# Kernel optimization log

Hardware: AMD Instinct MI355X
Metric: run time of the kernel (lower is better)

The kernel has to match this reference:

```python
import jax, jax.numpy as jnp
import numpy as np

N_NODES = 50000
N_EDGES = 800000
N_FEAT = 128
N_HID = 128
N_CLS = 40
BN_EPS = 1e-5


def setup_inputs() -> dict:
    key = jax.random.key(0)
    ks = jax.random.split(key, 8)
    return {
        "x": jax.random.normal(ks[0], (N_NODES, N_FEAT), dtype=jnp.float32),
        "edge_index": jax.random.randint(ks[1], (2, N_EDGES), 0, N_NODES, dtype=jnp.int64),
        "W1l": jax.random.normal(ks[2], (N_HID, N_FEAT), dtype=jnp.float32) / np.sqrt(N_FEAT),
        "b1": jnp.zeros((N_HID,), dtype=jnp.float32),
        "W1r": jax.random.normal(ks[3], (N_HID, N_FEAT), dtype=jnp.float32) / np.sqrt(N_FEAT),
        "gamma": jnp.ones((N_HID,), dtype=jnp.float32),
        "beta": jnp.zeros((N_HID,), dtype=jnp.float32),
        "run_mean": jax.random.normal(ks[4], (N_HID,), dtype=jnp.float32) * 0.1,
        "run_var": jax.random.uniform(ks[5], (N_HID,), dtype=jnp.float32) + 0.5,
        "W2l": jax.random.normal(ks[6], (N_CLS, N_HID), dtype=jnp.float32) / np.sqrt(N_HID),
        "b2": jnp.zeros((N_CLS,), dtype=jnp.float32),
        "W2r": jax.random.normal(ks[7], (N_CLS, N_HID), dtype=jnp.float32) / np.sqrt(N_HID),
    }


def _sage_conv(h, src, dst, n_nodes, inv_deg, Wl, bl, Wr):
    # mean-aggregate neighbor features at each destination node
    agg = jax.ops.segment_sum(h[src], dst, num_segments=n_nodes)  # [N, D]
    agg = agg * inv_deg[:, None]
    # PyG SAGEConv: lin_l(aggr) (with bias) + lin_r(x) (no bias)
    return agg @ Wl.T + bl + h @ Wr.T


def reference(x, edge_index, W1l, b1, W1r, gamma, beta, run_mean, run_var, W2l, b2, W2r):
    src, dst = edge_index[0], edge_index[1]
    n = x.shape[0]
    deg = jax.ops.segment_sum(jnp.ones_like(src, dtype=x.dtype), dst, num_segments=n)
    inv_deg = 1.0 / jnp.maximum(deg, 1.0)
    h = _sage_conv(x, src, dst, n, inv_deg, W1l, b1, W1r)
    # transition: ReLU -> BatchNorm1d (eval: running stats) -> Dropout (identity in eval)
    h = jnp.maximum(h, 0.0)
    h = (h - run_mean) * (gamma / jnp.sqrt(run_var + BN_EPS)) + beta
    out = _sage_conv(h, src, dst, n, inv_deg, W2l, b2, W2r)
    return out
```

## Files before the change

### kernel.cpp

```cpp
#include <hip/hip_runtime.h>

#define N_NODES 50000
#define N_EDGES 800000
#define N_FEAT 128
#define N_HID 128
#define N_CLS 40
#define BN_EPS 1e-5f

#define CSR_STRIDE 64
#define NXCD 8
#define P_NODES 6250
#define CSR_B 2048
#define CSR_BO 256
#define WPACK_B 84
#define XPACK_B 3125
#define G2_SUB 51

typedef short bf16x8 __attribute__((ext_vector_type(8)));
typedef float f32x4 __attribute__((ext_vector_type(4)));

__device__ __forceinline__ unsigned bfpack(float a, float b) {
    unsigned ua = __float_as_uint(a), ub = __float_as_uint(b);
    ua = (ua + 0x7FFFu + ((ua >> 16) & 1u)) >> 16;
    ub = (ub + 0x7FFFu + ((ub >> 16) & 1u)) >> 16;
    return ua | (ub << 16);
}
__device__ __forceinline__ unsigned short bfr1(float a) {
    unsigned u = __float_as_uint(a);
    u = (u + 0x7FFFu + ((u >> 16) & 1u)) >> 16;
    return (unsigned short)u;
}
__device__ __forceinline__ float bflo(unsigned u) { return __uint_as_float(u << 16); }
__device__ __forceinline__ float bfhi(unsigned u) { return __uint_as_float(u & 0xFFFF0000u); }

__global__ __launch_bounds__(256) void degprep_kernel(
    const int* __restrict__ src, const int* __restrict__ dst,
    int* __restrict__ deg_i, unsigned short* __restrict__ csr_pad,
    const float* __restrict__ W1l, const float* __restrict__ W1r,
    const float* __restrict__ W2l, const float* __restrict__ W2r,
    const float* __restrict__ x, unsigned* __restrict__ WfA,
    unsigned* __restrict__ WfB, unsigned* __restrict__ x_bf16) {
    int b = blockIdx.x;
    int t = threadIdx.x;
    if (b < CSR_B) {
        const int p = b & (NXCD - 1);
        const int bo = b >> 3;
        const int plo = p * P_NODES;
        const int phi = plo + P_NODES;
        const int4* dst4 = (const int4*)dst;
        const int4* src4 = (const int4*)src;
        for (int c = bo; c * 1024 < N_EDGES; c += CSR_BO) {
            int e = c * 1024 + t * 4;
            if (e < N_EDGES) {
                int i4 = e >> 2;
                int4 d4 = dst4[i4];
                bool k0 = (d4.x >= plo) && (d4.x < phi);
                bool k1 = (d4.y >= plo) && (d4.y < phi);
                bool k2 = (d4.z >= plo) && (d4.z < phi);
                bool k3 = (d4.w >= plo) && (d4.w < phi);
                if (k0 | k1 | k2 | k3) {
                    int4 s4 = src4[i4];
                    if (k0) { int r = atomicAdd(&deg_i[d4.x], 1);
                        if (r < CSR_STRIDE) csr_pad[d4.x * CSR_STRIDE + r] = (unsigned short)s4.x; }
                    if (k1) { int r = atomicAdd(&deg_i[d4.y], 1);
                        if (r < CSR_STRIDE) csr_pad[d4.y * CSR_STRIDE + r] = (unsigned short)s4.y; }
                    if (k2) { int r = atomicAdd(&deg_i[d4.z], 1);
                        if (r < CSR_STRIDE) csr_pad[d4.z * CSR_STRIDE + r] = (unsigned short)s4.z; }
                    if (k3) { int r = atomicAdd(&deg_i[d4.w], 1);
                        if (r < CSR_STRIDE) csr_pad[d4.w * CSR_STRIDE + r] = (unsigned short)s4.w; }
                }
            }
        }
        return;
    }
    int i = (b - CSR_B) * 256 + t;
    if (b < CSR_B + WPACK_B) {
        if (i < 16384) {
            int f = i >> 8, r = i & 255;
            int lane = r >> 2, u = r & 3;
            int phase = f >> 5, kc = (f >> 3) & 3, nt = f & 7;
            int k0 = phase * 128 + kc * 32 + (lane >> 4) * 8 + u * 2;
            int n = nt * 16 + (lane & 15);
            float w0, w1;
            if (k0 < 128) {
                w0 = W1l[n * 128 + k0];
                w1 = W1l[n * 128 + k0 + 1];
            } else {
                w0 = W1r[n * 128 + k0 - 128];
                w1 = W1r[n * 128 + k0 - 127];
            }
            WfA[i] = bfpack(w0, w1);
        } else if (i < 21504) {
            int j = i - 16384;
            int f = j >> 8, r = j & 255;
            int lane = r >> 2, u = r & 3;
            int kc = f / 5, nt = f % 5;
            int k0 = kc * 32 + (lane >> 4) * 8 + u * 2;
            int n = nt * 16 + (lane & 15);
            float w0, w1;
            if (n < 40) {
                w0 = W2l[n * 128 + k0];
                w1 = W2l[n * 128 + k0 + 1];
            } else {
                w0 = W2r[(n - 40) * 128 + k0];
                w1 = W2r[(n - 40) * 128 + k0 + 1];
            }
            WfB[j] = bfpack(w0, w1);
        }
    } else {
        int j = (b - CSR_B - WPACK_B) * 256 + t;
        if (j < 800000) {
            const float4* xf = (const float4*)x;
            float4 a = xf[(size_t)j * 2];
            float4 bq = xf[(size_t)j * 2 + 1];
            uint4 o;
            o.x = bfpack(a.x, a.y);
            o.y = bfpack(a.z, a.w);
            o.z = bfpack(bq.x, bq.y);
            o.w = bfpack(bq.z, bq.w);
            ((uint4*)x_bf16)[j] = o;
        }
    }
}

__global__ __launch_bounds__(256) void gg_kernel(
    const unsigned short* __restrict__ csr_pad, const int* __restrict__ deg_i,
    const unsigned* __restrict__ x_bf16,
    const unsigned* __restrict__ WfA, const unsigned* __restrict__ WfB,
    const float* __restrict__ b1,
    const float* __restrict__ gamma, const float* __restrict__ beta,
    const float* __restrict__ rmean, const float* __restrict__ rvar,
    unsigned short* __restrict__ z2s, float* __restrict__ p2) {
    __shared__ unsigned Asu0[16 * 68];
    __shared__ unsigned Asu1[16 * 68];
    __shared__ __align__(16) unsigned short Cs[16 * 64];
    const int t = threadIdx.x;
    const int wid = __builtin_amdgcn_readfirstlane(t >> 6);
    const int lane = t & 63;
    const int li = lane & 15;
    const int quad = lane >> 4;
    const int sg = t >> 4;
    const int gl = t & 15;
    const int tb = blockIdx.x * 16;
    const uint4* xb4 = (const uint4*)x_bf16;

    uint4 xs = xb4[(size_t)(tb + sg) * 16 + gl];
    ((uint2*)Cs)[t] = ((const uint2*)(csr_pad + (size_t)tb * 64))[t];
    __syncthreads();

    int gid = tb + sg;
    int n = min(deg_i[gid], CSR_STRIDE);
    const unsigned short* cr = Cs + sg * 64;
    float acc[8];
#pragma unroll
    for (int j = 0; j < 8; ++j) acc[j] = 0.f;
    int k = 0;
    for (; k + 7 < n; k += 8) {
        uint4 tv[8];
#pragma unroll
        for (int q = 0; q < 8; ++q) {
            int s = cr[k + q];
            tv[q] = xb4[(size_t)s * 16 + gl];
        }
#pragma unroll
        for (int q = 0; q < 8; ++q) {
            acc[0] += bflo(tv[q].x); acc[1] += bfhi(tv[q].x);
            acc[2] += bflo(tv[q].y); acc[3] += bfhi(tv[q].y);
            acc[4] += bflo(tv[q].z); acc[5] += bfhi(tv[q].z);
            acc[6] += bflo(tv[q].w); acc[7] += bfhi(tv[q].w);
        }
    }
    if (k + 3 < n) {
        uint4 tv[4];
#pragma unroll
        for (int q = 0; q < 4; ++q) {
            int s = cr[k + q];
            tv[q] = xb4[(size_t)s * 16 + gl];
        }
#pragma unroll
        for (int q = 0; q < 4; ++q) {
            acc[0] += bflo(tv[q].x); acc[1] += bfhi(tv[q].x);
            acc[2] += bflo(tv[q].y); acc[3] += bfhi(tv[q].y);
            acc[4] += bflo(tv[q].z); acc[5] += bfhi(tv[q].z);
            acc[6] += bflo(tv[q].w); acc[7] += bfhi(tv[q].w);
        }
        k += 4;
    }
    for (; k < n; ++k) {
        int s = cr[k];
        uint4 t0 = xb4[(size_t)s * 16 + gl];
        acc[0] += bflo(t0.x); acc[1] += bfhi(t0.x);
        acc[2] += bflo(t0.y); acc[3] += bfhi(t0.y);
        acc[4] += bflo(t0.z); acc[5] += bfhi(t0.z);
        acc[6] += bflo(t0.w); acc[7] += bfhi(t0.w);
    }
    float inv = 1.0f / fmaxf((float)n, 1.0f);
    uint4 o;
    o.x = bfpack(acc[0] * inv, acc[1] * inv);
    o.y = bfpack(acc[2] * inv, acc[3] * inv);
    o.z = bfpack(acc[4] * inv, acc[5] * inv);
    o.w = bfpack(acc[6] * inv, acc[7] * inv);

    *(uint4*)&Asu1[sg * 68 + gl * 4] = xs;
    *(uint4*)&Asu0[sg * 68 + gl * 4] = o;
    __syncthreads();

    bf16x8 af0[4], af1[4];
#pragma unroll
    for (int kc = 0; kc < 4; ++kc) {
        af0[kc] = *(const bf16x8*)&Asu0[li * 68 + kc * 16 + quad * 4];
        af1[kc] = *(const bf16x8*)&Asu1[li * 68 + kc * 16 + quad * 4];
    }

    f32x4 dacc[2];
#pragma unroll
    for (int j = 0; j < 2; ++j) dacc[j] = (f32x4){0.f, 0.f, 0.f, 0.f};
#pragma unroll
    for (int j = 0; j < 2; ++j) {
        int nt = wid * 2 + j;
#pragma unroll
        for (int kc = 0; kc < 4; ++kc) {
            bf16x8 bfr = *(const bf16x8*)(WfA + (size_t)(kc * 8 + nt) * 256 + lane * 4);
            dacc[j] = __builtin_amdgcn_mfma_f32_16x16x32_bf16(af0[kc], bfr, dacc[j], 0, 0, 0);
        }
#pragma unroll
        for (int kc = 0; kc < 4; ++kc) {
            bf16x8 bfr = *(const bf16x8*)(WfA + 8192 + (size_t)(kc * 8 + nt) * 256 + lane * 4);
            dacc[j] = __builtin_amdgcn_mfma_f32_16x16x32_bf16(af1[kc], bfr, dacc[j], 0, 0, 0);
        }
    }
    __syncthreads();

    unsigned short* Hs = (unsigned short*)Asu0;
#pragma unroll
    for (int j = 0; j < 2; ++j) {
        int nt = wid * 2 + j;
        int cgc = nt * 16 + li;
        float sc = gamma[cgc] * rsqrtf(rvar[cgc] + BN_EPS);
        float sh = fmaf(-rmean[cgc], sc, beta[cgc]);
        float bb = b1[cgc];
#pragma unroll
        for (int r = 0; r < 4; ++r) {
            int row = quad * 4 + r;
            float pre = dacc[j][r] + bb;
            Hs[row * 136 + cgc] = bfr1(fmaf(fmaxf(pre, 0.f), sc, sh));
        }
    }
    __syncthreads();

    bf16x8 af2[4];
#pragma unroll
    for (int kc = 0; kc < 4; ++kc)
        af2[kc] = *(const bf16x8*)&Asu0[li * 68 + kc * 16 + quad * 4];

    int nNT = (wid == 0) ? 2 : 1;
    f32x4 d2[2];
#pragma unroll
    for (int j = 0; j < 2; ++j) d2[j] = (f32x4){0.f, 0.f, 0.f, 0.f};
    for (int j = 0; j < nNT; ++j) {
        int nt = (j == 0) ? wid : 4;
#pragma unroll
        for (int kc = 0; kc < 4; ++kc) {
            bf16x8 bfr = *(const bf16x8*)(WfB + (size_t)(kc * 5 + nt) * 256 + lane * 4);
            d2[j] = __builtin_amdgcn_mfma_f32_16x16x32_bf16(af2[kc], bfr, d2[j], 0, 0, 0);
        }
    }
    for (int j = 0; j < nNT; ++j) {
        int nt = (j == 0) ? wid : 4;
        int cgc = nt * 16 + li;
#pragma unroll
        for (int r = 0; r < 4; ++r) {
            int row = tb + quad * 4 + r;
            float vv = d2[j][r];
            if (cgc < 40) z2s[(size_t)row * 40 + cgc] = bfr1(vv);
            else p2[(size_t)row * 40 + (cgc - 40)] = vv;
        }
    }
}

__global__ __launch_bounds__(256) void gather2_kernel(const unsigned short* __restrict__ csr_pad,
                                                      const int* __restrict__ deg_i,
                                                      const unsigned short* __restrict__ z2s,
                                                      const float* __restrict__ p2,
                                                      const float* __restrict__ b2,
                                                      float* __restrict__ out) {
    __shared__ __align__(16) unsigned short Cs[G2_SUB * 64];
    int t = threadIdx.x;
    int nb_base = blockIdx.x * G2_SUB;
    int nn = min(G2_SUB, N_NODES - nb_base);
    int limit_u2 = (nn * 64) >> 2;
    const uint2* cg = (const uint2*)(csr_pad + (size_t)nb_base * 64);
    for (int i = t; i < limit_u2; i += 256) ((uint2*)Cs)[i] = cg[i];
    __syncthreads();

    int sub = t / 5;
    int li = t - sub * 5;
    if (sub >= G2_SUB) return;
    int gid = nb_base + sub;
    if (gid >= N_NODES) return;
    int n = min(deg_i[gid], CSR_STRIDE);
    const unsigned short* cr = Cs + sub * 64;
    const uint4* z4 = (const uint4*)z2s;
    float acc[8];
#pragma unroll
    for (int j = 0; j < 8; ++j) acc[j] = 0.f;
    int k = 0;
    for (; k + 7 < n; k += 8) {
        uint4 tv[8];
#pragma unroll
        for (int q = 0; q < 8; ++q) {
            int s = cr[k + q];
            tv[q] = z4[(size_t)s * 5 + li];
        }
#pragma unroll
        for (int q = 0; q < 8; ++q) {
            acc[0] += bflo(tv[q].x); acc[1] += bfhi(tv[q].x);
            acc[2] += bflo(tv[q].y); acc[3] += bfhi(tv[q].y);
            acc[4] += bflo(tv[q].z); acc[5] += bfhi(tv[q].z);
            acc[6] += bflo(tv[q].w); acc[7] += bfhi(tv[q].w);
        }
    }
    if (k + 3 < n) {
        uint4 tv[4];
#pragma unroll
        for (int q = 0; q < 4; ++q) {
            int s = cr[k + q];
            tv[q] = z4[(size_t)s * 5 + li];
        }
#pragma unroll
        for (int q = 0; q < 4; ++q) {
            acc[0] += bflo(tv[q].x); acc[1] += bfhi(tv[q].x);
            acc[2] += bflo(tv[q].y); acc[3] += bfhi(tv[q].y);
            acc[4] += bflo(tv[q].z); acc[5] += bfhi(tv[q].z);
            acc[6] += bflo(tv[q].w); acc[7] += bfhi(tv[q].w);
        }
        k += 4;
    }
    for (; k < n; ++k) {
        int s = cr[k];
        uint4 t0 = z4[(size_t)s * 5 + li];
        acc[0] += bflo(t0.x); acc[1] += bfhi(t0.x);
        acc[2] += bflo(t0.y); acc[3] += bfhi(t0.y);
        acc[4] += bflo(t0.z); acc[5] += bfhi(t0.z);
        acc[6] += bflo(t0.w); acc[7] += bfhi(t0.w);
    }
    float inv = 1.0f / fmaxf((float)n, 1.0f);
    const float4* p4 = (const float4*)p2;
    const float4* b4 = (const float4*)b2;
    float4 pa = p4[(size_t)gid * 10 + li * 2];
    float4 pb = p4[(size_t)gid * 10 + li * 2 + 1];
    float4 ba = b4[li * 2];
    float4 bb = b4[li * 2 + 1];
    float4 ra, rb;
    ra.x = fmaf(acc[0], inv, pa.x + ba.x);
    ra.y = fmaf(acc[1], inv, pa.y + ba.y);
    ra.z = fmaf(acc[2], inv, pa.z + ba.z);
    ra.w = fmaf(acc[3], inv, pa.w + ba.w);
    rb.x = fmaf(acc[4], inv, pb.x + bb.x);
    rb.y = fmaf(acc[5], inv, pb.y + bb.y);
    rb.z = fmaf(acc[6], inv, pb.z + bb.z);
    rb.w = fmaf(acc[7], inv, pb.w + bb.w);
    ((float4*)out)[(size_t)gid * 10 + li * 2] = ra;
    ((float4*)out)[(size_t)gid * 10 + li * 2 + 1] = rb;
}

extern "C" void kernel_launch(void* const* d_in, const int* in_sizes, int n_in,
                              void* d_out, int out_size, void* d_ws, size_t ws_size,
                              hipStream_t stream) {
    const float* x     = (const float*)d_in[0];
    const int*   ei    = (const int*)d_in[1];
    const float* W1l   = (const float*)d_in[2];
    const float* b1    = (const float*)d_in[3];
    const float* W1r   = (const float*)d_in[4];
    const float* gamma = (const float*)d_in[5];
    const float* beta  = (const float*)d_in[6];
    const float* rmean = (const float*)d_in[7];
    const float* rvar  = (const float*)d_in[8];
    const float* W2l   = (const float*)d_in[9];
    const float* b2    = (const float*)d_in[10];
    const float* W2r   = (const float*)d_in[11];
    float* out = (float*)d_out;

    int* deg_i              = (int*)d_ws;
    unsigned short* csr_pad = (unsigned short*)(deg_i + 50048);
    unsigned* WfA           = (unsigned*)(deg_i + 50048 + 1600000);
    unsigned* WfB           = WfA + 16384;
    unsigned* x_bf16        = WfB + 5120;
    unsigned short* z2s     = (unsigned short*)(x_bf16 + 3200000);
    float* p2               = (float*)(z2s + (size_t)50048 * 40);

    const int* src = ei;
    const int* dst = ei + N_EDGES;

    hipMemsetAsync(deg_i, 0, (size_t)50048 * sizeof(int), stream);

    degprep_kernel<<<CSR_B + WPACK_B + XPACK_B, 256, 0, stream>>>(
        src, dst, deg_i, csr_pad, W1l, W1r, W2l, W2r, x, WfA, WfB, x_bf16);

    gg_kernel<<<N_NODES / 16, 256, 0, stream>>>(
        csr_pad, deg_i, x_bf16, WfA, WfB, b1, gamma, beta, rmean, rvar, z2s, p2);

    gather2_kernel<<<(N_NODES + G2_SUB - 1) / G2_SUB, 256, 0, stream>>>(
        csr_pad, deg_i, z2s, p2, b2, out);
}
```

Baseline: 182.9 us.

## Build padded CSR via two-pass bucketed scatter with LDS-local atomics

Replaces the per-XCD-partitioned global-atomic CSR build with a two-phase approach. Edges are first bucketed by dst>>8 into 196 fixed-capacity record buffers using shared-memory histograms and one global atomic per bucket per block. A second kernel then builds each bucket's 256-node CSR slice in LDS and writes it out coalesced. The aim is to cut the global atomic traffic and scattered 2-byte writes, at the cost of an extra kernel launch, an intermediate record buffer, and a fixed bucket capacity that silently drops edges if a bucket overflows.

```diff
diff --git a/kernel.cpp b/kernel.cpp
--- a/kernel.cpp
+++ b/kernel.cpp
@@ -8,12 +8,12 @@
 #define BN_EPS 1e-5f
 
 #define CSR_STRIDE 64
-#define NXCD 8
-#define P_NODES 6250
-#define CSR_B 2048
-#define CSR_BO 256
-#define WPACK_B 84
-#define XPACK_B 3125
+#define NBKT 196
+#define REC_CAP 6144
+#define PA_B 196
+#define WPACK1K 21
+#define XPACK1K 782
+#define D1_B (PA_B + WPACK1K + XPACK1K)
 #define G2_SUB 51
 
 typedef short bf16x8 __attribute__((ext_vector_type(8)));
@@ -33,48 +33,50 @@
 __device__ __forceinline__ float bflo(unsigned u) { return __uint_as_float(u << 16); }
 __device__ __forceinline__ float bfhi(unsigned u) { return __uint_as_float(u & 0xFFFF0000u); }
 
-__global__ __launch_bounds__(256) void degprep_kernel(
+__global__ __launch_bounds__(1024) void d1_kernel(
     const int* __restrict__ src, const int* __restrict__ dst,
-    int* __restrict__ deg_i, unsigned short* __restrict__ csr_pad,
+    int* __restrict__ gcur, unsigned* __restrict__ rec,
     const float* __restrict__ W1l, const float* __restrict__ W1r,
     const float* __restrict__ W2l, const float* __restrict__ W2r,
     const float* __restrict__ x, unsigned* __restrict__ WfA,
     unsigned* __restrict__ WfB, unsigned* __restrict__ x_bf16) {
     int b = blockIdx.x;
     int t = threadIdx.x;
-    if (b < CSR_B) {
-        const int p = b & (NXCD - 1);
-        const int bo = b >> 3;
-        const int plo = p * P_NODES;
-        const int phi = plo + P_NODES;
-        const int4* dst4 = (const int4*)dst;
-        const int4* src4 = (const int4*)src;
-        for (int c = bo; c * 1024 < N_EDGES; c += CSR_BO) {
-            int e = c * 1024 + t * 4;
-            if (e < N_EDGES) {
-                int i4 = e >> 2;
-                int4 d4 = dst4[i4];
-                bool k0 = (d4.x >= plo) && (d4.x < phi);
-                bool k1 = (d4.y >= plo) && (d4.y < phi);
-                bool k2 = (d4.z >= plo) && (d4.z < phi);
-                bool k3 = (d4.w >= plo) && (d4.w < phi);
-                if (k0 | k1 | k2 | k3) {
-                    int4 s4 = src4[i4];
-                    if (k0) { int r = atomicAdd(&deg_i[d4.x], 1);
-                        if (r < CSR_STRIDE) csr_pad[d4.x * CSR_STRIDE + r] = (unsigned short)s4.x; }
-                    if (k1) { int r = atomicAdd(&deg_i[d4.y], 1);
-                        if (r < CSR_STRIDE) csr_pad[d4.y * CSR_STRIDE + r] = (unsigned short)s4.y; }
-                    if (k2) { int r = atomicAdd(&deg_i[d4.z], 1);
-                        if (r < CSR_STRIDE) csr_pad[d4.z * CSR_STRIDE + r] = (unsigned short)s4.z; }
-                    if (k3) { int r = atomicAdd(&deg_i[d4.w], 1);
-                        if (r < CSR_STRIDE) csr_pad[d4.w * CSR_STRIDE + r] = (unsigned short)s4.w; }
-                }
+    if (b < PA_B) {
+        __shared__ int hist[NBKT];
+        __shared__ int base[NBKT];
+        if (t < NBKT) hist[t] = 0;
+        __syncthreads();
+        int e = b * 4096 + t * 4;
+        bool val = e < N_EDGES;
+        int4 d4 = {0, 0, 0, 0}, s4 = {0, 0, 0, 0};
+        int bk[4], rk[4];
+        if (val) {
+            d4 = ((const int4*)dst)[e >> 2];
+            s4 = ((const int4*)src)[e >> 2];
+            bk[0] = d4.x >> 8; rk[0] = atomicAdd(&hist[bk[0]], 1);
+            bk[1] = d4.y >> 8; rk[1] = atomicAdd(&hist[bk[1]], 1);
+            bk[2] = d4.z >> 8; rk[2] = atomicAdd(&hist[bk[2]], 1);
+            bk[3] = d4.w >> 8; rk[3] = atomicAdd(&hist[bk[3]], 1);
+        }
+        __syncthreads();
+        if (t < NBKT) base[t] = atomicAdd(&gcur[t], hist[t]);
+        __syncthreads();
+        if (val) {
+            int dl[4] = {d4.x & 255, d4.y & 255, d4.z & 255, d4.w & 255};
+            int sv[4] = {s4.x, s4.y, s4.z, s4.w};
+#pragma unroll
+            for (int q = 0; q < 4; ++q) {
+                int pos = base[bk[q]] + rk[q];
+                if (pos < REC_CAP)
+                    rec[(size_t)bk[q] * REC_CAP + pos] =
+                        (unsigned)dl[q] | ((unsigned)sv[q] << 16);
             }
         }
         return;
     }
-    int i = (b - CSR_B) * 256 + t;
-    if (b < CSR_B + WPACK_B) {
+    if (b < PA_B + WPACK1K) {
+        int i = (b - PA_B) * 1024 + t;
         if (i < 16384) {
             int f = i >> 8, r = i & 255;
             int lane = r >> 2, u = r & 3;
@@ -108,7 +110,7 @@
             WfB[j] = bfpack(w0, w1);
         }
     } else {
-        int j = (b - CSR_B - WPACK_B) * 256 + t;
+        int j = (b - PA_B - WPACK1K) * 1024 + t;
         if (j < 800000) {
             const float4* xf = (const float4*)x;
             float4 a = xf[(size_t)j * 2];
@@ -121,6 +123,34 @@
             ((uint4*)x_bf16)[j] = o;
         }
     }
+}
+
+__global__ __launch_bounds__(256) void phaseB_kernel(
+    const int* __restrict__ gcur, const unsigned* __restrict__ rec,
+    int* __restrict__ deg_i, unsigned short* __restrict__ csr_pad) {
+    __shared__ __align__(16) unsigned short csr_l[256 * CSR_STRIDE];
+    __shared__ int deg_l[256];
+    int t = threadIdx.x;
+    int bid = blockIdx.x;
+    deg_l[t] = 0;
+    __syncthreads();
+    int nrec = min(gcur[bid], REC_CAP);
+    const unsigned* rb = rec + (size_t)bid * REC_CAP;
+    for (int i = t; i < nrec; i += 256) {
+        unsigned u = rb[i];
+        int nl = (int)(u & 255u);
+        unsigned short sv = (unsigned short)(u >> 16);
+        int r = atomicAdd(&deg_l[nl], 1);
+        if (r < CSR_STRIDE) csr_l[nl * CSR_STRIDE + r] = sv;
+    }
+    __syncthreads();
+    int nb = bid * 256;
+    int nn = min(256, N_NODES - nb);
+    if (t < nn) deg_i[nb + t] = deg_l[t];
+    int n_u4 = nn * (CSR_STRIDE / 8);
+    uint4* gout = (uint4*)(csr_pad + (size_t)nb * CSR_STRIDE);
+    const uint4* lin = (const uint4*)csr_l;
+    for (int i = t; i < n_u4; i += 256) gout[i] = lin[i];
 }
 
 __global__ __launch_bounds__(256) void gg_kernel(
@@ -381,7 +411,9 @@
     const float* W2r   = (const float*)d_in[11];
     float* out = (float*)d_out;
 
-    int* deg_i              = (int*)d_ws;
+    int* gcur               = (int*)d_ws;
+    unsigned* rec           = (unsigned*)(gcur + 256);
+    int* deg_i              = (int*)(rec + (size_t)NBKT * REC_CAP);
     unsigned short* csr_pad = (unsigned short*)(deg_i + 50048);
     unsigned* WfA           = (unsigned*)(deg_i + 50048 + 1600000);
     unsigned* WfB           = WfA + 16384;
@@ -392,10 +424,12 @@
     const int* src = ei;
     const int* dst = ei + N_EDGES;
 
-    hipMemsetAsync(deg_i, 0, (size_t)50048 * sizeof(int), stream);
-
-    degprep_kernel<<<CSR_B + WPACK_B + XPACK_B, 256, 0, stream>>>(
-        src, dst, deg_i, csr_pad, W1l, W1r, W2l, W2r, x, WfA, WfB, x_bf16);
+    hipMemsetAsync(gcur, 0, 256 * sizeof(int), stream);
+
+    d1_kernel<<<D1_B, 1024, 0, stream>>>(
+        src, dst, gcur, rec, W1l, W1r, W2l, W2r, x, WfA, WfB, x_bf16);
+
+    phaseB_kernel<<<NBKT, 256, 0, stream>>>(gcur, rec, deg_i, csr_pad);
 
     gg_kernel<<<N_NODES / 16, 256, 0, stream>>>(
         csr_pad, deg_i, x_bf16, WfA, WfB, b1, gamma, beta, rmean, rvar, z2s, p2);
```

New measurement: 159.2 us, median of 2. 13.0% less time.
